# Performance work log

Hardware: AMD Instinct MI355X
Metric: run time of the kernel (lower is better)

## Reference

```python
import jax, jax.numpy as jnp
import numpy as np

N_NODES = 50000
N_EDGES = 800000
D_IN = 96
D_HID = 96
D_OUT = 96


def _mean_agg(x, src, dst, n_nodes):
    # mean over in-neighbors: agg[v] = mean_{(u->v) in E} x[u]
    msg = x[src]  # [E, d] irregular gather
    summed = jax.ops.segment_sum(msg, dst, num_segments=n_nodes)  # [N, d]
    deg = jax.ops.segment_sum(jnp.ones((src.shape[0],), x.dtype), dst,
                              num_segments=n_nodes)  # [N]
    return summed / jnp.maximum(deg, 1.0)[:, None]


def _sage_conv(x, src, dst, W_self, W_neigh, b):
    agg = _mean_agg(x, src, dst, x.shape[0])
    return x @ W_self + agg @ W_neigh + b


def setup_inputs() -> dict:
    key = jax.random.key(0)
    ks = jax.random.split(key, 9)
    s = 0.05
    return {
        "x": jax.random.normal(ks[0], (N_NODES, D_IN), jnp.float32),
        "src": jax.random.randint(ks[1], (N_EDGES,), 0, N_NODES),
        "dst": jax.random.randint(ks[2], (N_EDGES,), 0, N_NODES),
        "W_self1": jax.random.normal(ks[3], (D_IN, D_HID), jnp.float32) * s,
        "W_neigh1": jax.random.normal(ks[4], (D_IN, D_HID), jnp.float32) * s,
        "b1": jnp.zeros((D_HID,), jnp.float32),
        "W_self2": jax.random.normal(ks[5], (D_HID, D_OUT), jnp.float32) * s,
        "W_neigh2": jax.random.normal(ks[6], (D_HID, D_OUT), jnp.float32) * s,
        "b2": jnp.zeros((D_OUT,), jnp.float32),
    }


def reference(x, src, dst, W_self1, W_neigh1, b1, W_self2, W_neigh2, b2):
    h = _sage_conv(x, src, dst, W_self1, W_neigh1, b1)
    h = jax.nn.relu(h)
    h = _sage_conv(h, src, dst, W_self2, W_neigh2, b2)
    return h
```

## Files before the change

### kernel.cpp

```cpp
#include <hip/hip_runtime.h>
#include <cstdint>
#include <cstddef>

#define NN 50000
#define NE 800000
#define D 96

#define NBUCK 512
#define BSH 7
#define NBU ((NN + 127) >> 7)
#define TILE 8192
#define NTILE ((NE + TILE - 1) / TILE)
#define MAXB 5120

#define AGB 32
#define AGW 1024

#define Q1f (3.0f / 127.0f)
#define INVQ1f (127.0f / 3.0f)
#define Q2f (1.6f / 127.0f)
#define INVQ2f (127.0f / 1.6f)

typedef __attribute__((ext_vector_type(8))) short bf16x8;
typedef __attribute__((ext_vector_type(4))) float f32x4;


__global__ void bucket_hist(const int* __restrict__ dst, int* __restrict__ bucketCnt) {
    __shared__ int h[NBUCK];
    for (int i = threadIdx.x; i < NBUCK; i += 256) h[i] = 0;
    __syncthreads();
    const int stride = gridDim.x * 256 * 4;
    for (int i = (blockIdx.x * 256 + (int)threadIdx.x) * 4; i < NE; i += stride) {
        int4 d4 = *(const int4*)(dst + i);
        atomicAdd(&h[d4.x >> BSH], 1);
        atomicAdd(&h[d4.y >> BSH], 1);
        atomicAdd(&h[d4.z >> BSH], 1);
        atomicAdd(&h[d4.w >> BSH], 1);
    }
    __syncthreads();
    for (int i = threadIdx.x; i < NBUCK; i += 256)
        if (h[i]) atomicAdd(&bucketCnt[i], h[i]);
}

__global__ void bucket_scan(const int* __restrict__ bucketCnt, int* __restrict__ bucketBase,
                            int* __restrict__ bucketCur) {
    __shared__ int sm[NBUCK];
    const int t = threadIdx.x;
    const int v = bucketCnt[t];
    sm[t] = v;
    __syncthreads();
    for (int s = 1; s < NBUCK; s <<= 1) {
        int u = (t >= s) ? sm[t - s] : 0;
        __syncthreads();
        sm[t] += u;
        __syncthreads();
    }
    const int excl = sm[t] - v;
    bucketBase[t] = excl;
    bucketCur[t] = excl;
}

__launch_bounds__(512)
__global__ void bin_edges(const int* __restrict__ dst, const int* __restrict__ src,
                          int* __restrict__ bucketCur, uint2* __restrict__ pairBuf) {
    __shared__ int hist[NBUCK];
    __shared__ int segStart[NBUCK];
    __shared__ int lcur[NBUCK];
    __shared__ int segBase[NBUCK];
    __shared__ uint2 lpair[TILE];
    const int t = threadIdx.x;
    const int e0 = blockIdx.x * TILE;
    const int cnt = (NE - e0 < TILE) ? (NE - e0) : TILE;

    for (int i = t; i < NBUCK; i += 512) hist[i] = 0;
    __syncthreads();

    for (int i = t * 4; i < cnt; i += 512 * 4) {
        if (i + 3 < cnt) {
            int4 d4 = *(const int4*)(dst + e0 + i);
            atomicAdd(&hist[d4.x >> BSH], 1);
            atomicAdd(&hist[d4.y >> BSH], 1);
            atomicAdd(&hist[d4.z >> BSH], 1);
            atomicAdd(&hist[d4.w >> BSH], 1);
        } else {
            for (int k = i; k < cnt; ++k) atomicAdd(&hist[dst[e0 + k] >> BSH], 1);
        }
    }
    __syncthreads();

    {
        const int v = hist[t];
        segStart[t] = v;
        __syncthreads();
        for (int s = 1; s < NBUCK; s <<= 1) {
            int u = (t >= s) ? segStart[t - s] : 0;
            __syncthreads();
            segStart[t] += u;
            __syncthreads();
        }
        int excl = segStart[t] - v;
        __syncthreads();
        segStart[t] = excl;
        lcur[t] = excl;
    }
    __syncthreads();

    for (int i = t * 4; i < cnt; i += 512 * 4) {
        if (i + 3 < cnt) {
            int4 d4 = *(const int4*)(dst + e0 + i);
            int4 s4 = *(const int4*)(src + e0 + i);
            int p0 = atomicAdd(&lcur[d4.x >> BSH], 1); lpair[p0] = make_uint2(d4.x, s4.x);
            int p1 = atomicAdd(&lcur[d4.y >> BSH], 1); lpair[p1] = make_uint2(d4.y, s4.y);
            int p2 = atomicAdd(&lcur[d4.z >> BSH], 1); lpair[p2] = make_uint2(d4.z, s4.z);
            int p3 = atomicAdd(&lcur[d4.w >> BSH], 1); lpair[p3] = make_uint2(d4.w, s4.w);
        } else {
            for (int k = i; k < cnt; ++k) {
                int d = dst[e0 + k], s = src[e0 + k];
                int p = atomicAdd(&lcur[d >> BSH], 1);
                lpair[p] = make_uint2(d, s);
            }
        }
    }
    __syncthreads();

    {
        int c = hist[t];
        segBase[t] = c ? atomicAdd(&bucketCur[t], c) : 0;
    }
    __syncthreads();

    for (int k = t; k < cnt; k += 512) {
        uint2 p = lpair[k];
        int b = (int)p.x >> BSH;
        pairBuf[(size_t)segBase[b] + (k - segStart[b])] = p;
    }
}

__global__ void csr_build(const uint2* __restrict__ pairBuf, const int* __restrict__ bucketBase,
                          const int* __restrict__ bucketCnt, int* __restrict__ startv,
                          int* __restrict__ csr) {
    __shared__ int h[128], ls[128], cur[128];
    __shared__ int lsrc[MAXB];
    const int b = blockIdx.x;
    const int t = threadIdx.x;
    const int lo = bucketBase[b];
    int cnt = bucketCnt[b];
    if (cnt > MAXB) cnt = MAXB;
    const int node0 = b << BSH;

    if (t < 128) h[t] = 0;
    __syncthreads();
    for (int k = t; k < cnt; k += 256)
        atomicAdd(&h[(int)pairBuf[lo + k].x - node0], 1);
    __syncthreads();
    if (t < 128) ls[t] = h[t];
    __syncthreads();
    for (int s = 1; s < 128; s <<= 1) {
        int u = (t >= s && t < 128) ? ls[t - s] : 0;
        __syncthreads();
        if (t < 128) ls[t] += u;
        __syncthreads();
    }
    if (t < 128) {
        int excl = ls[t] - h[t];
        cur[t] = excl;
        int node = node0 + t;
        if (node < NN) startv[node] = lo + excl;
    }
    __syncthreads();
    for (int k = t; k < cnt; k += 256) {
        uint2 p = pairBuf[lo + k];
        int pos = atomicAdd(&cur[(int)p.x - node0], 1);
        lsrc[pos] = (int)p.y;
    }
    __syncthreads();
    for (int k = t; k < cnt; k += 256) csr[lo + k] = lsrc[k];
}


__device__ inline uint32_t pack2_bf16(float a, float b) {
    uint32_t ua = __float_as_uint(a), ub = __float_as_uint(b);
    ua = (ua + 0x7fffu + ((ua >> 16) & 1u)) >> 16;
    ub = (ub + 0x7fffu + ((ub >> 16) & 1u)) >> 16;
    return ua | (ub << 16);
}

__device__ inline unsigned short pack1_bf16(float a) {
    uint32_t ua = __float_as_uint(a);
    return (unsigned short)((ua + 0x7fffu + ((ua >> 16) & 1u)) >> 16);
}

__device__ inline float bf_lo(uint32_t w) { return __uint_as_float(w << 16); }
__device__ inline float bf_hi(uint32_t w) { return __uint_as_float(w & 0xffff0000u); }

__device__ inline signed char q8(float v, float invq) {
    float s = v * invq;
    s = s > 127.f ? 127.f : (s < -127.f ? -127.f : s);
    return (signed char)__float2int_rn(s);
}


__global__ void repack_both(const float* __restrict__ Ws1, const float* __restrict__ Wn1,
                            const float* __restrict__ Ws2, const float* __restrict__ Wn2,
                            uint32_t* __restrict__ bfg1, uint32_t* __restrict__ bfg2) {
    int t = blockIdx.x * 256 + threadIdx.x;
    if (t >= 4608) return;
    const int layer = (t >= 2304);
    int tt = t - layer * 2304;
    const int isWn = (tt >= 1152);
    const float* __restrict__ W = layer ? (isWn ? Wn2 : Ws2) : (isWn ? Wn1 : Ws1);
    uint32_t* __restrict__ Bfg = layer ? bfg2 : bfg1;
    tt = isWn ? tt - 1152 : tt;
    int s = tt / 384;
    int r = tt - s * 384;
    int nt6 = r >> 6;
    int l = r & 63;
    int col = nt6 * 16 + (l & 15);
    int k0 = 32 * s + 8 * (l >> 4);
    float v[8];
#pragma unroll
    for (int j = 0; j < 8; ++j) v[j] = W[(k0 + j) * D + col];
    uint4 o;
    o.x = pack2_bf16(v[0], v[1]);
    o.y = pack2_bf16(v[2], v[3]);
    o.z = pack2_bf16(v[4], v[5]);
    o.w = pack2_bf16(v[6], v[7]);
    int nt = nt6 + (isWn ? 6 : 0);
    int slot = (s * 12 + nt) * 64 + l;
    *(uint4*)(Bfg + (size_t)slot * 4) = o;
}


__launch_bounds__(256, 2)
__global__ void xform1_mfma(const float* __restrict__ X,
                            const uint32_t* __restrict__ Bfg,
                            const float* __restrict__ Bias,
                            unsigned short* __restrict__ Ys,
                            signed char* __restrict__ Yn) {
    __shared__ __align__(16) uint32_t Af[3072];
    const int tid = threadIdx.x;
    const int row0 = blockIdx.x * 64;

#pragma unroll
    for (int it = 0; it < 6; ++it) {
        int flat = (it * 256 + tid) * 4;
        int r = flat / 96, k = flat - (flat / 96) * 96;
        int gr = row0 + r;
        if (gr >= NN) gr = NN - 1;
        float4 xv = *(const float4*)(X + (size_t)gr * D + k);
        int wq = r >> 4, s = k >> 5;
        int lq = ((k >> 3) & 3) * 16 + (r & 15);
        int base = ((wq * 3 + s) * 64 + lq) * 4 + ((k & 7) >> 1);
        Af[base] = pack2_bf16(xv.x, xv.y);
        Af[base + 1] = pack2_bf16(xv.z, xv.w);
    }
    __syncthreads();

    const int w = tid >> 6, l = tid & 63;
    const int cl = l & 15;

    bf16x8 a0 = *(const bf16x8*)&Af[((w * 3 + 0) * 64 + l) * 4];
    bf16x8 a1 = *(const bf16x8*)&Af[((w * 3 + 1) * 64 + l) * 4];
    bf16x8 a2 = *(const bf16x8*)&Af[((w * 3 + 2) * 64 + l) * 4];

    f32x4 acc[12];
#pragma unroll
    for (int nt = 0; nt < 6; ++nt) {
        float bv = Bias[nt * 16 + cl];
        acc[nt] = (f32x4){bv, bv, bv, bv};
    }
#pragma unroll
    for (int nt = 6; nt < 12; ++nt) acc[nt] = (f32x4){0.f, 0.f, 0.f, 0.f};

#pragma unroll
    for (int nt = 0; nt < 12; ++nt) {
        bf16x8 b0 = *(const bf16x8*)(Bfg + ((size_t)((0 * 12 + nt) * 64 + l)) * 4);
        bf16x8 b1 = *(const bf16x8*)(Bfg + ((size_t)((1 * 12 + nt) * 64 + l)) * 4);
        bf16x8 b2 = *(const bf16x8*)(Bfg + ((size_t)((2 * 12 + nt) * 64 + l)) * 4);
        acc[nt] = __builtin_amdgcn_mfma_f32_16x16x32_bf16(a0, b0, acc[nt], 0, 0, 0);
        acc[nt] = __builtin_amdgcn_mfma_f32_16x16x32_bf16(a1, b1, acc[nt], 0, 0, 0);
        acc[nt] = __builtin_amdgcn_mfma_f32_16x16x32_bf16(a2, b2, acc[nt], 0, 0, 0);
    }

    const int grb = row0 + w * 16 + (l >> 4) * 4;
#pragma unroll
    for (int nt = 0; nt < 6; ++nt)
#pragma unroll
        for (int rg = 0; rg < 4; ++rg) {
            int gr = grb + rg;
            if (gr < NN) Ys[(size_t)gr * D + nt * 16 + cl] = pack1_bf16(acc[nt][rg]);
        }
#pragma unroll
    for (int nt = 6; nt < 12; ++nt)
#pragma unroll
        for (int rg = 0; rg < 4; ++rg) {
            int gr = grb + rg;
            if (gr < NN) Yn[(size_t)gr * D + (nt - 6) * 16 + cl] = q8(acc[nt][rg], INVQ1f);
        }
}


#define GATHER_BODY_I8(TBL, GET)                                           \
    {                                                                      \
        int e = 0;                                                         \
        for (; e + 7 < dg; e += 8) {                                       \
            _Pragma("unroll")                                              \
            for (int i = 0; i < 8; ++i) {                                  \
                unsigned short wv = TBL[(size_t)(GET(e + i)) * 48 + li];   \
                sx[i] += (int)(signed char)(wv & 0xff);                    \
                sy[i] += (int)(signed char)(wv >> 8);                      \
            }                                                              \
        }                                                                  \
        if (e + 3 < dg) {                                                  \
            _Pragma("unroll")                                              \
            for (int i = 0; i < 4; ++i) {                                  \
                unsigned short wv = TBL[(size_t)(GET(e + i)) * 48 + li];   \
                sx[i] += (int)(signed char)(wv & 0xff);                    \
                sy[i] += (int)(signed char)(wv >> 8);                      \
            }                                                              \
            e += 4;                                                        \
        }                                                                  \
        for (; e < dg; ++e) {                                              \
            unsigned short wv = TBL[(size_t)(GET(e)) * 48 + li];           \
            sx[0] += (int)(signed char)(wv & 0xff);                        \
            sy[0] += (int)(signed char)(wv >> 8);                          \
        }                                                                  \
    }


__launch_bounds__(256, 6)
__global__ void fused_aggx(const unsigned short* __restrict__ Ys1,
                           const unsigned short* __restrict__ Yn1,
                           const int* __restrict__ csr, const int* __restrict__ startv,
                           const uint32_t* __restrict__ Bfg2, const float* __restrict__ Bias2,
                           unsigned short* __restrict__ Ys2, signed char* __restrict__ Yn2) {
    __shared__ __align__(16) uint32_t H[AGB][52];
    __shared__ int lcsr[AGW];
    __shared__ int lsv[AGB + 1];
    const int tid = threadIdx.x;
    const int w = tid >> 6, l = tid & 63;
    const int row0 = blockIdx.x * AGB;
    const int li = (l < 48) ? l : 0;

    if (tid <= AGB) {
        int r = row0 + tid;
        lsv[tid] = (r < NN) ? startv[r] : NE;
    }
    __syncthreads();
    const int e_lo = lsv[0];
    const int wcnt = lsv[AGB] - e_lo;
    const int staged = wcnt < AGW ? wcnt : AGW;
    for (int k = tid; k < staged; k += 256) lcsr[k] = csr[e_lo + k];
    __syncthreads();

    for (int j = 0; j < 8; ++j) {
        const int vl = w * 8 + j;
        const int v = row0 + vl;
        uint32_t hpair = 0;
        if (v < NN) {
            const int sloc = lsv[vl] - e_lo;
            const int dg = lsv[vl + 1] - lsv[vl];
            int sx[8], sy[8];
#pragma unroll
            for (int i = 0; i < 8; ++i) { sx[i] = 0; sy[i] = 0; }
            if (sloc + dg <= staged) {
#define GET_L(E) lcsr[sloc + (E)]
                GATHER_BODY_I8(Yn1, GET_L)
#undef GET_L
            } else {
                const int* cp = csr + e_lo + sloc;
#define GET_G(E) cp[E]
                GATHER_BODY_I8(Yn1, GET_G)
#undef GET_G
            }
            int axi = ((sx[0] + sx[1]) + (sx[2] + sx[3])) + ((sx[4] + sx[5]) + (sx[6] + sx[7]));
            int ayi = ((sy[0] + sy[1]) + (sy[2] + sy[3])) + ((sy[4] + sy[5]) + (sy[6] + sy[7]));
            const float inv = Q1f / (float)(dg > 0 ? dg : 1);
            uint32_t ysp = *(const uint32_t*)(Ys1 + (size_t)v * 96 + 2 * li);
            float r0 = fmaxf(bf_lo(ysp) + (float)axi * inv, 0.f);
            float r1 = fmaxf(bf_hi(ysp) + (float)ayi * inv, 0.f);
            hpair = pack2_bf16(r0, r1);
        }
        if (l < 48) H[vl][l] = hpair;
    }
    __syncthreads();

    const int stripe = w >> 1;
    const int hf = w & 1;
    const int cl = l & 15;
    const int kq = l >> 4;

    bf16x8 a0 = *(const bf16x8*)&H[stripe * 16 + cl][0 + 4 * kq];
    bf16x8 a1 = *(const bf16x8*)&H[stripe * 16 + cl][16 + 4 * kq];
    bf16x8 a2 = *(const bf16x8*)&H[stripe * 16 + cl][32 + 4 * kq];

    f32x4 acc[6];
#pragma unroll
    for (int nt = 0; nt < 6; ++nt) {
        float bv = hf ? 0.f : Bias2[nt * 16 + cl];
        acc[nt] = (f32x4){bv, bv, bv, bv};
    }
#pragma unroll
    for (int nt = 0; nt < 6; ++nt) {
        int ntg = hf * 6 + nt;
        bf16x8 b0 = *(const bf16x8*)(Bfg2 + ((size_t)((0 * 12 + ntg) * 64 + l)) * 4);
        bf16x8 b1 = *(const bf16x8*)(Bfg2 + ((size_t)((1 * 12 + ntg) * 64 + l)) * 4);
        bf16x8 b2 = *(const bf16x8*)(Bfg2 + ((size_t)((2 * 12 + ntg) * 64 + l)) * 4);
        acc[nt] = __builtin_amdgcn_mfma_f32_16x16x32_bf16(a0, b0, acc[nt], 0, 0, 0);
        acc[nt] = __builtin_amdgcn_mfma_f32_16x16x32_bf16(a1, b1, acc[nt], 0, 0, 0);
        acc[nt] = __builtin_amdgcn_mfma_f32_16x16x32_bf16(a2, b2, acc[nt], 0, 0, 0);
    }

    const int grb = row0 + stripe * 16 + kq * 4;
    if (hf == 0) {
#pragma unroll
        for (int nt = 0; nt < 6; ++nt)
#pragma unroll
            for (int rg = 0; rg < 4; ++rg) {
                int gr = grb + rg;
                if (gr < NN) Ys2[(size_t)gr * D + nt * 16 + cl] = pack1_bf16(acc[nt][rg]);
            }
    } else {
#pragma unroll
        for (int nt = 0; nt < 6; ++nt)
#pragma unroll
            for (int rg = 0; rg < 4; ++rg) {
                int gr = grb + rg;
                if (gr < NN) Yn2[(size_t)gr * D + nt * 16 + cl] = q8(acc[nt][rg], INVQ2f);
            }
    }
}


__launch_bounds__(256, 8)
__global__ void agg_final(const unsigned short* __restrict__ Ys2b,
                          const unsigned short* __restrict__ Yn2,
                          const int* __restrict__ csr, const int* __restrict__ startv,
                          float* __restrict__ out) {
    __shared__ int lcsr[AGW];
    __shared__ int lsv[AGB + 1];
    const int tid = threadIdx.x;
    const int w = tid >> 6, l = tid & 63;
    const int row0 = blockIdx.x * AGB;
    const int li = (l < 48) ? l : 0;

    if (tid <= AGB) {
        int r = row0 + tid;
        lsv[tid] = (r < NN) ? startv[r] : NE;
    }
    __syncthreads();
    const int e_lo = lsv[0];
    const int wcnt = lsv[AGB] - e_lo;
    const int staged = wcnt < AGW ? wcnt : AGW;
    for (int k = tid; k < staged; k += 256) lcsr[k] = csr[e_lo + k];
    __syncthreads();

    for (int j = 0; j < 8; ++j) {
        const int vl = w * 8 + j;
        const int v = row0 + vl;
        if (v >= NN) continue;
        const int sloc = lsv[vl] - e_lo;
        const int dg = lsv[vl + 1] - lsv[vl];
        int sx[8], sy[8];
#pragma unroll
        for (int i = 0; i < 8; ++i) { sx[i] = 0; sy[i] = 0; }
        if (sloc + dg <= staged) {
#define GET_L(E) lcsr[sloc + (E)]
            GATHER_BODY_I8(Yn2, GET_L)
#undef GET_L
        } else {
            const int* cp = csr + e_lo + sloc;
#define GET_G(E) cp[E]
            GATHER_BODY_I8(Yn2, GET_G)
#undef GET_G
        }
        int axi = ((sx[0] + sx[1]) + (sx[2] + sx[3])) + ((sx[4] + sx[5]) + (sx[6] + sx[7]));
        int ayi = ((sy[0] + sy[1]) + (sy[2] + sy[3])) + ((sy[4] + sy[5]) + (sy[6] + sy[7]));
        const float inv = Q2f / (float)(dg > 0 ? dg : 1);
        if (l < 48) {
            const size_t o = (size_t)v * D + 2 * li;
            uint32_t ysp = *(const uint32_t*)(Ys2b + (size_t)v * 96 + 2 * li);
            out[o] = bf_lo(ysp) + (float)axi * inv;
            out[o + 1] = bf_hi(ysp) + (float)ayi * inv;
        }
    }
}


extern "C" void kernel_launch(void* const* d_in, const int* in_sizes, int n_in,
                              void* d_out, int out_size, void* d_ws, size_t ws_size,
                              hipStream_t stream) {
    const float* x   = (const float*)d_in[0];
    const int*   src = (const int*)d_in[1];
    const int*   dst = (const int*)d_in[2];
    const float* Ws1 = (const float*)d_in[3];
    const float* Wn1 = (const float*)d_in[4];
    const float* b1  = (const float*)d_in[5];
    const float* Ws2 = (const float*)d_in[6];
    const float* Wn2 = (const float*)d_in[7];
    const float* b2  = (const float*)d_in[8];
    float* out = (float*)d_out;

    char* w = (char*)d_ws;
    int* startv     = (int*)w; w += (size_t)NN * sizeof(int);
    int* bucketCnt  = (int*)w; w += NBUCK * sizeof(int);
    int* bucketBase = (int*)w; w += NBUCK * sizeof(int);
    int* bucketCur  = (int*)w; w += NBUCK * sizeof(int);
    int* csr        = (int*)w; w += (size_t)NE * sizeof(int);
    w = (char*)(((uintptr_t)w + 255) & ~(uintptr_t)255);
    unsigned short* ys1 = (unsigned short*)w; w += (size_t)NN * D * sizeof(unsigned short);
    unsigned short* ys2 = (unsigned short*)w; w += (size_t)NN * D * sizeof(unsigned short);
    signed char*    yn1 = (signed char*)w;    w += (size_t)NN * D;
    signed char*    yn2 = (signed char*)w;    w += (size_t)NN * D;
    w = (char*)(((uintptr_t)w + 255) & ~(uintptr_t)255);
    uint32_t* bfg1 = (uint32_t*)w; w += 36 * 64 * 4 * sizeof(uint32_t);
    uint32_t* bfg2 = (uint32_t*)w; w += 36 * 64 * 4 * sizeof(uint32_t);

    uint2* pairBuf = (uint2*)ys1;

    hipMemsetAsync(bucketCnt, 0, NBUCK * sizeof(int), stream);
    bucket_hist<<<256, 256, 0, stream>>>(dst, bucketCnt);
    bucket_scan<<<1, NBUCK, 0, stream>>>(bucketCnt, bucketBase, bucketCur);
    bin_edges<<<NTILE, 512, 0, stream>>>(dst, src, bucketCur, pairBuf);
    csr_build<<<NBU, 256, 0, stream>>>(pairBuf, bucketBase, bucketCnt, startv, csr);

    repack_both<<<18, 256, 0, stream>>>(Ws1, Wn1, Ws2, Wn2, bfg1, bfg2);

    xform1_mfma<<<(NN + 63) / 64, 256, 0, stream>>>(x, bfg1, b1, ys1, yn1);

    const int agrid = (NN + AGB - 1) / AGB;

    fused_aggx<<<agrid, 256, 0, stream>>>(ys1, (const unsigned short*)yn1, csr, startv,
                                          bfg2, b2, ys2, yn2);

    agg_final<<<agrid, 256, 0, stream>>>(ys2, (const unsigned short*)yn2, csr, startv, out);
}
```

Baseline: 105.9 us.

## Split wavefront into four edge groups with 8-byte int8 gathers and shuffle reduction

The neighbor gather in both aggregation kernels changes its thread mapping. Before, 48 lanes each loaded 2 bytes per edge and walked all edges serially. Now the 64 lanes form 4 groups of 16. Each group takes every fourth edge, and 12 lanes per group load 8 bytes each. Partial sums are combined with xor shuffles, and lane group 0 writes vectorized outputs (uint4 bf16 loads, float4 stores). The aim is to quadruple memory-level parallelism per wave and widen loads for low-degree nodes. The cost is masked lanes, shuffle overhead and 4 idle lanes per group.

```diff
diff --git a/kernel.cpp b/kernel.cpp
--- a/kernel.cpp
+++ b/kernel.cpp
@@ -300,37 +300,42 @@
 }
 
 
-#define GATHER_BODY_I8(TBL, GET)                                           \
-    {                                                                      \
-        int e = 0;                                                         \
-        for (; e + 7 < dg; e += 8) {                                       \
-            _Pragma("unroll")                                              \
-            for (int i = 0; i < 8; ++i) {                                  \
-                unsigned short wv = TBL[(size_t)(GET(e + i)) * 48 + li];   \
-                sx[i] += (int)(signed char)(wv & 0xff);                    \
-                sy[i] += (int)(signed char)(wv >> 8);                      \
-            }                                                              \
-        }                                                                  \
-        if (e + 3 < dg) {                                                  \
-            _Pragma("unroll")                                              \
-            for (int i = 0; i < 4; ++i) {                                  \
-                unsigned short wv = TBL[(size_t)(GET(e + i)) * 48 + li];   \
-                sx[i] += (int)(signed char)(wv & 0xff);                    \
-                sy[i] += (int)(signed char)(wv >> 8);                      \
-            }                                                              \
-            e += 4;                                                        \
-        }                                                                  \
-        for (; e < dg; ++e) {                                              \
-            unsigned short wv = TBL[(size_t)(GET(e)) * 48 + li];           \
-            sx[0] += (int)(signed char)(wv & 0xff);                        \
-            sy[0] += (int)(signed char)(wv >> 8);                          \
-        }                                                                  \
-    }
+#define GATHER4_I8(TBL, IDX)                                                \
+    {                                                                       \
+        const int nb = (dg + 3) >> 2;                                       \
+        _Pragma("unroll 4")                                                 \
+        for (int b = 0; b < nb; ++b) {                                      \
+            int ei = b * 4 + g;                                             \
+            int ec = ei < dg ? ei : dg - 1;                                 \
+            uint32_t mm = ei < dg ? 0xFFFFFFFFu : 0u;                       \
+            int rowi = IDX(ec);                                             \
+            uint2 vv = *(const uint2*)(TBL + (size_t)rowi * 96 + rr * 8);   \
+            vv.x &= mm; vv.y &= mm;                                         \
+            s0 += (int)(signed char)(vv.x);                                 \
+            s1 += (int)(signed char)(vv.x >> 8);                            \
+            s2 += (int)(signed char)(vv.x >> 16);                           \
+            s3 += (int)(signed char)(vv.x >> 24);                           \
+            s4 += (int)(signed char)(vv.y);                                 \
+            s5 += (int)(signed char)(vv.y >> 8);                            \
+            s6 += (int)(signed char)(vv.y >> 16);                           \
+            s7 += (int)(signed char)(vv.y >> 24);                           \
+        }                                                                   \
+    }
+
+#define REDUCE_XG()                                                         \
+    s0 += __shfl_xor(s0, 16); s0 += __shfl_xor(s0, 32);                     \
+    s1 += __shfl_xor(s1, 16); s1 += __shfl_xor(s1, 32);                     \
+    s2 += __shfl_xor(s2, 16); s2 += __shfl_xor(s2, 32);                     \
+    s3 += __shfl_xor(s3, 16); s3 += __shfl_xor(s3, 32);                     \
+    s4 += __shfl_xor(s4, 16); s4 += __shfl_xor(s4, 32);                     \
+    s5 += __shfl_xor(s5, 16); s5 += __shfl_xor(s5, 32);                     \
+    s6 += __shfl_xor(s6, 16); s6 += __shfl_xor(s6, 32);                     \
+    s7 += __shfl_xor(s7, 16); s7 += __shfl_xor(s7, 32);
 
 
 __launch_bounds__(256, 6)
 __global__ void fused_aggx(const unsigned short* __restrict__ Ys1,
-                           const unsigned short* __restrict__ Yn1,
+                           const signed char* __restrict__ Yn1,
                            const int* __restrict__ csr, const int* __restrict__ startv,
                            const uint32_t* __restrict__ Bfg2, const float* __restrict__ Bias2,
                            unsigned short* __restrict__ Ys2, signed char* __restrict__ Yn2) {
@@ -340,11 +345,13 @@
     const int tid = threadIdx.x;
     const int w = tid >> 6, l = tid & 63;
     const int row0 = blockIdx.x * AGB;
-    const int li = (l < 48) ? l : 0;
+    const int g = l >> 4;
+    const int r = l & 15;
+    const int rr = (r < 12) ? r : 0;
 
     if (tid <= AGB) {
-        int r = row0 + tid;
-        lsv[tid] = (r < NN) ? startv[r] : NE;
+        int rn = row0 + tid;
+        lsv[tid] = (rn < NN) ? startv[rn] : NE;
     }
     __syncthreads();
     const int e_lo = lsv[0];
@@ -356,32 +363,44 @@
     for (int j = 0; j < 8; ++j) {
         const int vl = w * 8 + j;
         const int v = row0 + vl;
-        uint32_t hpair = 0;
+        int s0 = 0, s1 = 0, s2 = 0, s3 = 0, s4 = 0, s5 = 0, s6 = 0, s7 = 0;
+        int dg = 0, sloc = 0;
         if (v < NN) {
-            const int sloc = lsv[vl] - e_lo;
-            const int dg = lsv[vl + 1] - lsv[vl];
-            int sx[8], sy[8];
-#pragma unroll
-            for (int i = 0; i < 8; ++i) { sx[i] = 0; sy[i] = 0; }
-            if (sloc + dg <= staged) {
+            sloc = lsv[vl] - e_lo;
+            dg = lsv[vl + 1] - lsv[vl];
+        }
+        if (sloc + dg <= staged) {
 #define GET_L(E) lcsr[sloc + (E)]
-                GATHER_BODY_I8(Yn1, GET_L)
+            GATHER4_I8(Yn1, GET_L)
 #undef GET_L
+        } else {
+            const int* cp = csr + e_lo + sloc;
+#define GET_G(E) cp[E]
+            GATHER4_I8(Yn1, GET_G)
+#undef GET_G
+        }
+        REDUCE_XG()
+        if (g == 0 && r < 12) {
+            if (v < NN) {
+                const float inv = Q1f / (float)(dg > 0 ? dg : 1);
+                uint4 ysq = *(const uint4*)(Ys1 + (size_t)v * 96 + r * 8);
+                float h0 = fmaxf(bf_lo(ysq.x) + (float)s0 * inv, 0.f);
+                float h1 = fmaxf(bf_hi(ysq.x) + (float)s1 * inv, 0.f);
+                float h2 = fmaxf(bf_lo(ysq.y) + (float)s2 * inv, 0.f);
+                float h3 = fmaxf(bf_hi(ysq.y) + (float)s3 * inv, 0.f);
+                float h4 = fmaxf(bf_lo(ysq.z) + (float)s4 * inv, 0.f);
+                float h5 = fmaxf(bf_hi(ysq.z) + (float)s5 * inv, 0.f);
+                float h6 = fmaxf(bf_lo(ysq.w) + (float)s6 * inv, 0.f);
+                float h7 = fmaxf(bf_hi(ysq.w) + (float)s7 * inv, 0.f);
+                H[vl][r * 4 + 0] = pack2_bf16(h0, h1);
+                H[vl][r * 4 + 1] = pack2_bf16(h2, h3);
+                H[vl][r * 4 + 2] = pack2_bf16(h4, h5);
+                H[vl][r * 4 + 3] = pack2_bf16(h6, h7);
             } else {
-                const int* cp = csr + e_lo + sloc;
-#define GET_G(E) cp[E]
-                GATHER_BODY_I8(Yn1, GET_G)
-#undef GET_G
+                H[vl][r * 4 + 0] = 0; H[vl][r * 4 + 1] = 0;
+                H[vl][r * 4 + 2] = 0; H[vl][r * 4 + 3] = 0;
             }
-            int axi = ((sx[0] + sx[1]) + (sx[2] + sx[3])) + ((sx[4] + sx[5]) + (sx[6] + sx[7]));
-            int ayi = ((sy[0] + sy[1]) + (sy[2] + sy[3])) + ((sy[4] + sy[5]) + (sy[6] + sy[7]));
-            const float inv = Q1f / (float)(dg > 0 ? dg : 1);
-            uint32_t ysp = *(const uint32_t*)(Ys1 + (size_t)v * 96 + 2 * li);
-            float r0 = fmaxf(bf_lo(ysp) + (float)axi * inv, 0.f);
-            float r1 = fmaxf(bf_hi(ysp) + (float)ayi * inv, 0.f);
-            hpair = pack2_bf16(r0, r1);
-        }
-        if (l < 48) H[vl][l] = hpair;
+        }
     }
     __syncthreads();
 
@@ -434,7 +453,7 @@
 
 __launch_bounds__(256, 8)
 __global__ void agg_final(const unsigned short* __restrict__ Ys2b,
-                          const unsigned short* __restrict__ Yn2,
+                          const signed char* __restrict__ Yn2,
                           const int* __restrict__ csr, const int* __restrict__ startv,
                           float* __restrict__ out) {
     __shared__ int lcsr[AGW];
@@ -442,11 +461,13 @@
     const int tid = threadIdx.x;
     const int w = tid >> 6, l = tid & 63;
     const int row0 = blockIdx.x * AGB;
-    const int li = (l < 48) ? l : 0;
+    const int g = l >> 4;
+    const int r = l & 15;
+    const int rr = (r < 12) ? r : 0;
 
     if (tid <= AGB) {
-        int r = row0 + tid;
-        lsv[tid] = (r < NN) ? startv[r] : NE;
+        int rn = row0 + tid;
+        lsv[tid] = (rn < NN) ? startv[rn] : NE;
     }
     __syncthreads();
     const int e_lo = lsv[0];
@@ -461,27 +482,33 @@
         if (v >= NN) continue;
         const int sloc = lsv[vl] - e_lo;
         const int dg = lsv[vl + 1] - lsv[vl];
-        int sx[8], sy[8];
-#pragma unroll
-        for (int i = 0; i < 8; ++i) { sx[i] = 0; sy[i] = 0; }
+        int s0 = 0, s1 = 0, s2 = 0, s3 = 0, s4 = 0, s5 = 0, s6 = 0, s7 = 0;
         if (sloc + dg <= staged) {
 #define GET_L(E) lcsr[sloc + (E)]
-            GATHER_BODY_I8(Yn2, GET_L)
+            GATHER4_I8(Yn2, GET_L)
 #undef GET_L
         } else {
             const int* cp = csr + e_lo + sloc;
 #define GET_G(E) cp[E]
-            GATHER_BODY_I8(Yn2, GET_G)
+            GATHER4_I8(Yn2, GET_G)
 #undef GET_G
         }
-        int axi = ((sx[0] + sx[1]) + (sx[2] + sx[3])) + ((sx[4] + sx[5]) + (sx[6] + sx[7]));
-        int ayi = ((sy[0] + sy[1]) + (sy[2] + sy[3])) + ((sy[4] + sy[5]) + (sy[6] + sy[7]));
-        const float inv = Q2f / (float)(dg > 0 ? dg : 1);
-        if (l < 48) {
-            const size_t o = (size_t)v * D + 2 * li;
-            uint32_t ysp = *(const uint32_t*)(Ys2b + (size_t)v * 96 + 2 * li);
-            out[o] = bf_lo(ysp) + (float)axi * inv;
-            out[o + 1] = bf_hi(ysp) + (float)ayi * inv;
+        REDUCE_XG()
+        if (g == 0 && r < 12) {
+            const float inv = Q2f / (float)(dg > 0 ? dg : 1);
+            uint4 ysq = *(const uint4*)(Ys2b + (size_t)v * 96 + r * 8);
+            float4 o0, o1;
+            o0.x = bf_lo(ysq.x) + (float)s0 * inv;
+            o0.y = bf_hi(ysq.x) + (float)s1 * inv;
+            o0.z = bf_lo(ysq.y) + (float)s2 * inv;
+            o0.w = bf_hi(ysq.y) + (float)s3 * inv;
+            o1.x = bf_lo(ysq.z) + (float)s4 * inv;
+            o1.y = bf_hi(ysq.z) + (float)s5 * inv;
+            o1.z = bf_lo(ysq.w) + (float)s6 * inv;
+            o1.w = bf_hi(ysq.w) + (float)s7 * inv;
+            float* op = out + (size_t)v * D + r * 8;
+            *(float4*)(op) = o0;
+            *(float4*)(op + 4) = o1;
         }
     }
 }
@@ -510,8 +537,8 @@
     w = (char*)(((uintptr_t)w + 255) & ~(uintptr_t)255);
     unsigned short* ys1 = (unsigned short*)w; w += (size_t)NN * D * sizeof(unsigned short);
     unsigned short* ys2 = (unsigned short*)w; w += (size_t)NN * D * sizeof(unsigned short);
-    signed char*    yn1 = (signed char*)w;    w += (size_t)NN * D;
-    signed char*    yn2 = (signed char*)w;    w += (size_t)NN * D;
+    signed char*    yn1 = (signed char*)w;    w += (size_t)NN * D + 256;
+    signed char*    yn2 = (signed char*)w;    w += (size_t)NN * D + 256;
     w = (char*)(((uintptr_t)w + 255) & ~(uintptr_t)255);
     uint32_t* bfg1 = (uint32_t*)w; w += 36 * 64 * 4 * sizeof(uint32_t);
     uint32_t* bfg2 = (uint32_t*)w; w += 36 * 64 * 4 * sizeof(uint32_t);
@@ -530,8 +557,7 @@
 
     const int agrid = (NN + AGB - 1) / AGB;
 
-    fused_aggx<<<agrid, 256, 0, stream>>>(ys1, (const unsigned short*)yn1, csr, startv,
-                                          bfg2, b2, ys2, yn2);
-
-    agg_final<<<agrid, 256, 0, stream>>>(ys2, (const unsigned short*)yn2, csr, startv, out);
-}
+    fused_aggx<<<agrid, 256, 0, stream>>>(ys1, yn1, csr, startv, bfg2, b2, ys2, yn2);
+
+    agg_final<<<agrid, 256, 0, stream>>>(ys2, yn2, csr, startv, out);
+}
```

Result: slower. 121.6 us (+14.9%).

## Split neighbor gathers by source half to improve cache locality across two passes

Applied to the files above, without the earlier changes.

Each node's CSR neighbor list is partitioned by whether the source index falls below or above a split point, and a split offset is recorded per node. Every aggregation now runs as two kernels: the first gathers from the lower half of source rows and writes integer partial sums to a workspace buffer, and the second gathers the upper half and adds the partials. The intent is to shrink the gathered table's working set per pass so it fits better in L2/LLC. The cost is two extra kernel launches, a 19 MB partial-sum write and read per layer, and a second pass over the CSR.

```diff
diff --git a/kernel.cpp b/kernel.cpp
--- a/kernel.cpp
+++ b/kernel.cpp
@@ -5,6 +5,7 @@
 #define NN 50000
 #define NE 800000
 #define D 96
+#define NSPLIT 25000
 
 #define NBUCK 512
 #define BSH 7
@@ -138,8 +139,8 @@
 
 __global__ void csr_build(const uint2* __restrict__ pairBuf, const int* __restrict__ bucketBase,
                           const int* __restrict__ bucketCnt, int* __restrict__ startv,
-                          int* __restrict__ csr) {
-    __shared__ int h[128], ls[128], cur[128];
+                          int* __restrict__ splitv, int* __restrict__ csr) {
+    __shared__ int h[256], ls[256], cur[256];
     __shared__ int lsrc[MAXB];
     const int b = blockIdx.x;
     const int t = threadIdx.x;
@@ -148,29 +149,35 @@
     if (cnt > MAXB) cnt = MAXB;
     const int node0 = b << BSH;
 
-    if (t < 128) h[t] = 0;
-    __syncthreads();
-    for (int k = t; k < cnt; k += 256)
-        atomicAdd(&h[(int)pairBuf[lo + k].x - node0], 1);
-    __syncthreads();
-    if (t < 128) ls[t] = h[t];
-    __syncthreads();
-    for (int s = 1; s < 128; s <<= 1) {
-        int u = (t >= s && t < 128) ? ls[t - s] : 0;
+    h[t] = 0;
+    __syncthreads();
+    for (int k = t; k < cnt; k += 256) {
+        uint2 p = pairBuf[lo + k];
+        atomicAdd(&h[((int)p.x - node0) * 2 + ((int)p.y >= NSPLIT)], 1);
+    }
+    __syncthreads();
+    ls[t] = h[t];
+    __syncthreads();
+    for (int s = 1; s < 256; s <<= 1) {
+        int u = (t >= s) ? ls[t - s] : 0;
         __syncthreads();
-        if (t < 128) ls[t] += u;
+        ls[t] += u;
         __syncthreads();
     }
-    if (t < 128) {
+    {
         int excl = ls[t] - h[t];
         cur[t] = excl;
-        int node = node0 + t;
-        if (node < NN) startv[node] = lo + excl;
+        int node = node0 + (t >> 1);
+        if (node < NN) {
+            if ((t & 1) == 0) startv[node] = lo + excl;
+            else splitv[node] = lo + excl;
+        }
     }
     __syncthreads();
     for (int k = t; k < cnt; k += 256) {
         uint2 p = pairBuf[lo + k];
-        int pos = atomicAdd(&cur[(int)p.x - node0], 1);
+        int key = ((int)p.x - node0) * 2 + ((int)p.y >= NSPLIT);
+        int pos = atomicAdd(&cur[key], 1);
         lsrc[pos] = (int)p.y;
     }
     __syncthreads();
@@ -328,15 +335,13 @@
     }
 
 
-__launch_bounds__(256, 6)
-__global__ void fused_aggx(const unsigned short* __restrict__ Ys1,
-                           const unsigned short* __restrict__ Yn1,
-                           const int* __restrict__ csr, const int* __restrict__ startv,
-                           const uint32_t* __restrict__ Bfg2, const float* __restrict__ Bias2,
-                           unsigned short* __restrict__ Ys2, signed char* __restrict__ Yn2) {
-    __shared__ __align__(16) uint32_t H[AGB][52];
+__launch_bounds__(256, 8)
+__global__ void agg_p0(const unsigned short* __restrict__ Yn,
+                       const int* __restrict__ csr, const int* __restrict__ startv,
+                       const int* __restrict__ splitv, int2* __restrict__ P) {
     __shared__ int lcsr[AGW];
     __shared__ int lsv[AGB + 1];
+    __shared__ int lsp[AGB];
     const int tid = threadIdx.x;
     const int w = tid >> 6, l = tid & 63;
     const int row0 = blockIdx.x * AGB;
@@ -345,6 +350,67 @@
     if (tid <= AGB) {
         int r = row0 + tid;
         lsv[tid] = (r < NN) ? startv[r] : NE;
+    }
+    if (tid < AGB) {
+        int r = row0 + tid;
+        lsp[tid] = (r < NN) ? splitv[r] : NE;
+    }
+    __syncthreads();
+    const int e_lo = lsv[0];
+    const int wcnt = lsv[AGB] - e_lo;
+    const int staged = wcnt < AGW ? wcnt : AGW;
+    for (int k = tid; k < staged; k += 256) lcsr[k] = csr[e_lo + k];
+    __syncthreads();
+
+    for (int j = 0; j < 8; ++j) {
+        const int vl = w * 8 + j;
+        const int v = row0 + vl;
+        if (v >= NN) continue;
+        const int sloc = lsv[vl] - e_lo;
+        const int dg = lsp[vl] - lsv[vl];
+        int sx[8], sy[8];
+#pragma unroll
+        for (int i = 0; i < 8; ++i) { sx[i] = 0; sy[i] = 0; }
+        if (sloc + dg <= staged) {
+#define GET_L(E) lcsr[sloc + (E)]
+            GATHER_BODY_I8(Yn, GET_L)
+#undef GET_L
+        } else {
+            const int* cp = csr + e_lo + sloc;
+#define GET_G(E) cp[E]
+            GATHER_BODY_I8(Yn, GET_G)
+#undef GET_G
+        }
+        int axi = ((sx[0] + sx[1]) + (sx[2] + sx[3])) + ((sx[4] + sx[5]) + (sx[6] + sx[7]));
+        int ayi = ((sy[0] + sy[1]) + (sy[2] + sy[3])) + ((sy[4] + sy[5]) + (sy[6] + sy[7]));
+        if (l < 48) P[(size_t)v * 48 + li] = make_int2(axi, ayi);
+    }
+}
+
+
+__launch_bounds__(256, 6)
+__global__ void fused_aggx_p1(const unsigned short* __restrict__ Ys1,
+                              const unsigned short* __restrict__ Yn1,
+                              const int* __restrict__ csr, const int* __restrict__ startv,
+                              const int* __restrict__ splitv, const int2* __restrict__ P,
+                              const uint32_t* __restrict__ Bfg2, const float* __restrict__ Bias2,
+                              unsigned short* __restrict__ Ys2, signed char* __restrict__ Yn2) {
+    __shared__ __align__(16) uint32_t H[AGB][52];
+    __shared__ int lcsr[AGW];
+    __shared__ int lsv[AGB + 1];
+    __shared__ int lsp[AGB];
+    const int tid = threadIdx.x;
+    const int w = tid >> 6, l = tid & 63;
+    const int row0 = blockIdx.x * AGB;
+    const int li = (l < 48) ? l : 0;
+
+    if (tid <= AGB) {
+        int r = row0 + tid;
+        lsv[tid] = (r < NN) ? startv[r] : NE;
+    }
+    if (tid < AGB) {
+        int r = row0 + tid;
+        lsp[tid] = (r < NN) ? splitv[r] : NE;
     }
     __syncthreads();
     const int e_lo = lsv[0];
@@ -358,8 +424,9 @@
         const int v = row0 + vl;
         uint32_t hpair = 0;
         if (v < NN) {
-            const int sloc = lsv[vl] - e_lo;
-            const int dg = lsv[vl + 1] - lsv[vl];
+            const int sloc = lsp[vl] - e_lo;
+            const int dg = lsv[vl + 1] - lsp[vl];
+            const int dgT = lsv[vl + 1] - lsv[vl];
             int sx[8], sy[8];
 #pragma unroll
             for (int i = 0; i < 8; ++i) { sx[i] = 0; sy[i] = 0; }
@@ -373,9 +440,10 @@
                 GATHER_BODY_I8(Yn1, GET_G)
 #undef GET_G
             }
-            int axi = ((sx[0] + sx[1]) + (sx[2] + sx[3])) + ((sx[4] + sx[5]) + (sx[6] + sx[7]));
-            int ayi = ((sy[0] + sy[1]) + (sy[2] + sy[3])) + ((sy[4] + sy[5]) + (sy[6] + sy[7]));
-            const float inv = Q1f / (float)(dg > 0 ? dg : 1);
+            int2 pp = P[(size_t)v * 48 + li];
+            int axi = pp.x + ((sx[0] + sx[1]) + (sx[2] + sx[3])) + ((sx[4] + sx[5]) + (sx[6] + sx[7]));
+            int ayi = pp.y + ((sy[0] + sy[1]) + (sy[2] + sy[3])) + ((sy[4] + sy[5]) + (sy[6] + sy[7]));
+            const float inv = Q1f / (float)(dgT > 0 ? dgT : 1);
             uint32_t ysp = *(const uint32_t*)(Ys1 + (size_t)v * 96 + 2 * li);
             float r0 = fmaxf(bf_lo(ysp) + (float)axi * inv, 0.f);
             float r1 = fmaxf(bf_hi(ysp) + (float)ayi * inv, 0.f);
@@ -433,12 +501,14 @@
 
 
 __launch_bounds__(256, 8)
-__global__ void agg_final(const unsigned short* __restrict__ Ys2b,
-                          const unsigned short* __restrict__ Yn2,
-                          const int* __restrict__ csr, const int* __restrict__ startv,
-                          float* __restrict__ out) {
+__global__ void agg_final_p1(const unsigned short* __restrict__ Ys2b,
+                             const unsigned short* __restrict__ Yn2,
+                             const int* __restrict__ csr, const int* __restrict__ startv,
+                             const int* __restrict__ splitv, const int2* __restrict__ P,
+                             float* __restrict__ out) {
     __shared__ int lcsr[AGW];
     __shared__ int lsv[AGB + 1];
+    __shared__ int lsp[AGB];
     const int tid = threadIdx.x;
     const int w = tid >> 6, l = tid & 63;
     const int row0 = blockIdx.x * AGB;
@@ -448,6 +518,10 @@
         int r = row0 + tid;
         lsv[tid] = (r < NN) ? startv[r] : NE;
     }
+    if (tid < AGB) {
+        int r = row0 + tid;
+        lsp[tid] = (r < NN) ? splitv[r] : NE;
+    }
     __syncthreads();
     const int e_lo = lsv[0];
     const int wcnt = lsv[AGB] - e_lo;
@@ -459,8 +533,9 @@
         const int vl = w * 8 + j;
         const int v = row0 + vl;
         if (v >= NN) continue;
-        const int sloc = lsv[vl] - e_lo;
-        const int dg = lsv[vl + 1] - lsv[vl];
+        const int sloc = lsp[vl] - e_lo;
+        const int dg = lsv[vl + 1] - lsp[vl];
+        const int dgT = lsv[vl + 1] - lsv[vl];
         int sx[8], sy[8];
 #pragma unroll
         for (int i = 0; i < 8; ++i) { sx[i] = 0; sy[i] = 0; }
@@ -474,9 +549,10 @@
             GATHER_BODY_I8(Yn2, GET_G)
 #undef GET_G
         }
-        int axi = ((sx[0] + sx[1]) + (sx[2] + sx[3])) + ((sx[4] + sx[5]) + (sx[6] + sx[7]));
-        int ayi = ((sy[0] + sy[1]) + (sy[2] + sy[3])) + ((sy[4] + sy[5]) + (sy[6] + sy[7]));
-        const float inv = Q2f / (float)(dg > 0 ? dg : 1);
+        int2 pp = P[(size_t)v * 48 + li];
+        int axi = pp.x + ((sx[0] + sx[1]) + (sx[2] + sx[3])) + ((sx[4] + sx[5]) + (sx[6] + sx[7]));
+        int ayi = pp.y + ((sy[0] + sy[1]) + (sy[2] + sy[3])) + ((sy[4] + sy[5]) + (sy[6] + sy[7]));
+        const float inv = Q2f / (float)(dgT > 0 ? dgT : 1);
         if (l < 48) {
             const size_t o = (size_t)v * D + 2 * li;
             uint32_t ysp = *(const uint32_t*)(Ys2b + (size_t)v * 96 + 2 * li);
@@ -503,6 +579,7 @@
 
     char* w = (char*)d_ws;
     int* startv     = (int*)w; w += (size_t)NN * sizeof(int);
+    int* splitv     = (int*)w; w += (size_t)NN * sizeof(int);
     int* bucketCnt  = (int*)w; w += NBUCK * sizeof(int);
     int* bucketBase = (int*)w; w += NBUCK * sizeof(int);
     int* bucketCur  = (int*)w; w += NBUCK * sizeof(int);
@@ -510,9 +587,10 @@
     w = (char*)(((uintptr_t)w + 255) & ~(uintptr_t)255);
     unsigned short* ys1 = (unsigned short*)w; w += (size_t)NN * D * sizeof(unsigned short);
     unsigned short* ys2 = (unsigned short*)w; w += (size_t)NN * D * sizeof(unsigned short);
-    signed char*    yn1 = (signed char*)w;    w += (size_t)NN * D;
-    signed char*    yn2 = (signed char*)w;    w += (size_t)NN * D;
+    signed char*    yn1 = (signed char*)w;    w += (size_t)NN * D + 256;
+    signed char*    yn2 = (signed char*)w;    w += (size_t)NN * D + 256;
     w = (char*)(((uintptr_t)w + 255) & ~(uintptr_t)255);
+    int2* P = (int2*)w; w += (size_t)NN * 48 * sizeof(int2);
     uint32_t* bfg1 = (uint32_t*)w; w += 36 * 64 * 4 * sizeof(uint32_t);
     uint32_t* bfg2 = (uint32_t*)w; w += 36 * 64 * 4 * sizeof(uint32_t);
 
@@ -522,7 +600,7 @@
     bucket_hist<<<256, 256, 0, stream>>>(dst, bucketCnt);
     bucket_scan<<<1, NBUCK, 0, stream>>>(bucketCnt, bucketBase, bucketCur);
     bin_edges<<<NTILE, 512, 0, stream>>>(dst, src, bucketCur, pairBuf);
-    csr_build<<<NBU, 256, 0, stream>>>(pairBuf, bucketBase, bucketCnt, startv, csr);
+    csr_build<<<NBU, 256, 0, stream>>>(pairBuf, bucketBase, bucketCnt, startv, splitv, csr);
 
     repack_both<<<18, 256, 0, stream>>>(Ws1, Wn1, Ws2, Wn2, bfg1, bfg2);
 
@@ -530,8 +608,11 @@
 
     const int agrid = (NN + AGB - 1) / AGB;
 
-    fused_aggx<<<agrid, 256, 0, stream>>>(ys1, (const unsigned short*)yn1, csr, startv,
-                                          bfg2, b2, ys2, yn2);
-
-    agg_final<<<agrid, 256, 0, stream>>>(ys2, (const unsigned short*)yn2, csr, startv, out);
-}
+    agg_p0<<<agrid, 256, 0, stream>>>((const unsigned short*)yn1, csr, startv, splitv, P);
+    fused_aggx_p1<<<agrid, 256, 0, stream>>>(ys1, (const unsigned short*)yn1, csr, startv,
+                                             splitv, P, bfg2, b2, ys2, yn2);
+
+    agg_p0<<<agrid, 256, 0, stream>>>((const unsigned short*)yn2, csr, startv, splitv, P);
+    agg_final_p1<<<agrid, 256, 0, stream>>>(ys2, (const unsigned short*)yn2, csr, startv,
+                                            splitv, P, out);
+}
```

Result: slower. 129.0 us (+21.8%).
